# Performance work log

Measured on AMD Instinct MI355X. Metric: run time of the kernel, lower is better.

## Reference

```python
import jax, jax.numpy as jnp
import numpy as np

V_MIN = -10.0
V_MAX = 10.0
NUM_ATOMS = 51
ATOM_DELTA = (V_MAX - V_MIN) / (NUM_ATOMS - 1)
BS = 1_000_000


def setup_inputs() -> dict:
    key = jax.random.key(0)
    k1, k2 = jax.random.split(key)
    reward = jax.random.normal(k1, (BS,), dtype=jnp.float32) * 3.0
    probs = jax.random.uniform(k2, (BS, NUM_ATOMS), dtype=jnp.float32)
    atom_values = (V_MIN + ATOM_DELTA * jnp.arange(NUM_ATOMS)).astype(jnp.float32)
    return {"reward": reward, "probs": probs, "atom_values": atom_values}


def reference(reward, probs, atom_values):
    # Categorical (C51) Bellman projection, expressed as a scatter-add
    # instead of the original's dense [bs, A, A] projection matrix + bmm.
    bs, A = probs.shape
    # shifted & clamped atom support: [bs, A]
    new_vals = jnp.clip(atom_values[None, :] + reward[:, None], V_MIN, V_MAX)
    idx = (new_vals - V_MIN) / ATOM_DELTA           # fractional atom index
    lower = jnp.floor(idx)
    upper = jnp.ceil(idx)
    same = lower == upper                           # idx landed exactly on an atom
    l_coef = jnp.where(same, 1.0, upper - idx)      # original sets 1.0 when l == u
    u_coef = idx - lower                            # 0 when same
    li = lower.astype(jnp.int32)
    ui = upper.astype(jnp.int32)
    rows = jnp.broadcast_to(jnp.arange(bs)[:, None], (bs, A))
    out = jnp.zeros_like(probs)
    out = out.at[rows, li].add(l_coef * probs)
    out = out.at[rows, ui].add(u_coef * probs)
    return out
```

## Files before the change

### kernel.cpp

```cpp
#include <hip/hip_runtime.h>

#define NA 51
#define ROWS 64
#define GUARD 56
#define NDATA (ROWS * NA)
#define KCLAMP 52

__global__ __launch_bounds__(ROWS, 3) void c51_bellman_kernel(
    const float* __restrict__ reward,
    const float* __restrict__ probs,
    float* __restrict__ out,
    int bs)
{
    __shared__ float lds[GUARD + NDATA + GUARD];
    float* data = lds + GUARD;
    const int tid   = threadIdx.x;
    const int row0  = blockIdx.x * ROWS;
    const int nrows = min(ROWS, bs - row0);

    float s = 0.0f;
    if (tid < nrows) s = reward[row0 + tid] * 2.5f;

    if (nrows == ROWS) {
        const char* src = (const char*)(probs + (size_t)row0 * NA);
        #pragma unroll
        for (int t = 0; t < 12; ++t) {
            __builtin_amdgcn_global_load_lds(
                (const __attribute__((address_space(1))) void*)
                    (unsigned long long)(src + t * 1024 + tid * 16),
                (__attribute__((address_space(3))) void*)
                    (unsigned long long)(data + t * 256),
                16, 0, 0);
        }
        if (tid < 48) {
            const float4 v = *(const float4*)(src + 12288 + (size_t)tid * 16);
            *(float4*)(data + 3072 + tid * 4) = v;
        }
    } else {
        const int nelem = nrows * NA;
        for (int e = tid; e < nelem; e += ROWS)
            data[e] = probs[(size_t)row0 * NA + e];
    }
    asm volatile("s_waitcnt vmcnt(0) lgkmcnt(0)" ::: "memory");
    __builtin_amdgcn_sched_barrier(0);

    if (tid < nrows) {
        const float kf = floorf(s);
        const float f  = s - kf;
        int k = (int)kf;
        k = min(max(k, -KCLAMP), KCLAMP);

        const float* rp = data + tid * NA;

        float m_lo = 0.0f, m_hi = 0.0f;
        #pragma unroll
        for (int j = 0; j < NA; ++j) {
            const float pj = rp[j];
            const float t  = (float)j + s;
            if (t < 0.0f)  m_lo += pj;
            if (t > 50.0f) m_hi += pj;
        }

        const float* wb = data + tid * NA - k - 1;
        float w[52];
        #pragma unroll
        for (int m = 0; m < 52; ++m) w[m] = wb[m];

        float* wp = data + tid * NA;
        const float w1 = 1.0f - f;
        float prev = ((unsigned)(-k - 1) <= 50u) ? w[0] : 0.0f;
        #pragma unroll
        for (int i = 0; i < NA; ++i) {
            const float cur = ((unsigned)(i - k) <= 50u) ? w[i + 1] : 0.0f;
            float o;
            if (i == 0)           o = w1 * cur + m_lo;
            else if (i == NA - 1) o = ((f == 0.0f) ? cur : f * prev) + m_hi;
            else                  o = w1 * cur + f * prev;
            wp[i] = o;
            prev = cur;
        }
    }
    asm volatile("s_waitcnt lgkmcnt(0)" ::: "memory");
    __builtin_amdgcn_sched_barrier(0);

    if (nrows == ROWS) {
        float4* o4 = (float4*)(out + (size_t)row0 * NA);
        const float4* l4 = (const float4*)data;
        #pragma unroll
        for (int t = 0; t < 12; ++t) o4[t * 64 + tid] = l4[t * 64 + tid];
        if (tid < 48) o4[768 + tid] = l4[768 + tid];
    } else {
        const int nelem = nrows * NA;
        for (int e = tid; e < nelem; e += ROWS)
            out[(size_t)row0 * NA + e] = data[e];
    }
}

extern "C" void kernel_launch(void* const* d_in, const int* in_sizes, int n_in,
                              void* d_out, int out_size, void* d_ws, size_t ws_size,
                              hipStream_t stream) {
    const float* reward = (const float*)d_in[0];
    const float* probs  = (const float*)d_in[1];
    float* out = (float*)d_out;
    const int bs = in_sizes[0];

    const int blocks = (bs + ROWS - 1) / ROWS;
    c51_bellman_kernel<<<blocks, ROWS, 0, stream>>>(reward, probs, out, bs);
}
```

Measured before the change: 344.7 us.

## Drop LDS staging; load rows directly per thread and store nontemporally

```diff
diff --git a/kernel.cpp b/kernel.cpp
--- a/kernel.cpp
+++ b/kernel.cpp
@@ -1,99 +1,74 @@
 #include <hip/hip_runtime.h>
 
 #define NA 51
-#define ROWS 64
-#define GUARD 56
-#define NDATA (ROWS * NA)
+#define TPB 256
 #define KCLAMP 52
 
-__global__ __launch_bounds__(ROWS, 3) void c51_bellman_kernel(
+typedef float f4 __attribute__((ext_vector_type(4), aligned(4)));
+typedef float f2 __attribute__((ext_vector_type(2), aligned(4)));
+
+__global__ __launch_bounds__(TPB, 4) void c51_bellman_kernel(
     const float* __restrict__ reward,
     const float* __restrict__ probs,
     float* __restrict__ out,
     int bs)
 {
-    __shared__ float lds[GUARD + NDATA + GUARD];
-    float* data = lds + GUARD;
-    const int tid   = threadIdx.x;
-    const int row0  = blockIdx.x * ROWS;
-    const int nrows = min(ROWS, bs - row0);
+    const int r = blockIdx.x * TPB + threadIdx.x;
+    const bool edge = (blockIdx.x == 0) | (blockIdx.x == (int)gridDim.x - 1);
+    if (r >= bs) return;
 
-    float s = 0.0f;
-    if (tid < nrows) s = reward[row0 + tid] * 2.5f;
+    const float s  = reward[r] * 2.5f;
+    const float kf = floorf(s);
+    const float f  = s - kf;
+    int k = (int)kf;
+    k = min(max(k, -KCLAMP), KCLAMP);
 
-    if (nrows == ROWS) {
-        const char* src = (const char*)(probs + (size_t)row0 * NA);
+    const float* rp = probs + (size_t)r * NA;
+
+    float row[51];
+    #pragma unroll
+    for (int m = 0; m < 12; ++m) *(f4*)&row[4 * m] = *(const f4*)&rp[4 * m];
+    *(f2*)&row[48] = *(const f2*)&rp[48];
+    row[50] = rp[50];
+
+    float m_lo = 0.0f, m_hi = 0.0f;
+    #pragma unroll
+    for (int j = 0; j < NA; ++j) {
+        const float t = (float)j + s;
+        if (t < 0.0f)  m_lo += row[j];
+        if (t > 50.0f) m_hi += row[j];
+    }
+
+    float w[52];
+    if (!edge) {
+        const float* wb = rp - k - 1;
         #pragma unroll
-        for (int t = 0; t < 12; ++t) {
-            __builtin_amdgcn_global_load_lds(
-                (const __attribute__((address_space(1))) void*)
-                    (unsigned long long)(src + t * 1024 + tid * 16),
-                (__attribute__((address_space(3))) void*)
-                    (unsigned long long)(data + t * 256),
-                16, 0, 0);
-        }
-        if (tid < 48) {
-            const float4 v = *(const float4*)(src + 12288 + (size_t)tid * 16);
-            *(float4*)(data + 3072 + tid * 4) = v;
-        }
+        for (int m = 0; m < 13; ++m) *(f4*)&w[4 * m] = *(const f4*)&wb[4 * m];
     } else {
-        const int nelem = nrows * NA;
-        for (int e = tid; e < nelem; e += ROWS)
-            data[e] = probs[(size_t)row0 * NA + e];
+        #pragma unroll
+        for (int m = 0; m < 52; ++m)
+            w[m] = rp[min(max(m - k - 1, 0), NA - 1)];
     }
-    asm volatile("s_waitcnt vmcnt(0) lgkmcnt(0)" ::: "memory");
-    __builtin_amdgcn_sched_barrier(0);
 
-    if (tid < nrows) {
-        const float kf = floorf(s);
-        const float f  = s - kf;
-        int k = (int)kf;
-        k = min(max(k, -KCLAMP), KCLAMP);
+    const float w1 = 1.0f - f;
+    float prev = ((unsigned)(-k - 1) <= 50u) ? w[0] : 0.0f;
+    #pragma unroll
+    for (int i = 0; i < NA; ++i) {
+        const float cur = ((unsigned)(i - k) <= 50u) ? w[i + 1] : 0.0f;
+        float o;
+        if (i == 0)           o = w1 * cur + m_lo;
+        else if (i == NA - 1) o = ((f == 0.0f) ? cur : f * prev) + m_hi;
+        else                  o = w1 * cur + f * prev;
+        w[i] = o;
+        prev = cur;
+    }
 
-        const float* rp = data + tid * NA;
-
-        float m_lo = 0.0f, m_hi = 0.0f;
-        #pragma unroll
-        for (int j = 0; j < NA; ++j) {
-            const float pj = rp[j];
-            const float t  = (float)j + s;
-            if (t < 0.0f)  m_lo += pj;
-            if (t > 50.0f) m_hi += pj;
-        }
-
-        const float* wb = data + tid * NA - k - 1;
-        float w[52];
-        #pragma unroll
-        for (int m = 0; m < 52; ++m) w[m] = wb[m];
-
-        float* wp = data + tid * NA;
-        const float w1 = 1.0f - f;
-        float prev = ((unsigned)(-k - 1) <= 50u) ? w[0] : 0.0f;
-        #pragma unroll
-        for (int i = 0; i < NA; ++i) {
-            const float cur = ((unsigned)(i - k) <= 50u) ? w[i + 1] : 0.0f;
-            float o;
-            if (i == 0)           o = w1 * cur + m_lo;
-            else if (i == NA - 1) o = ((f == 0.0f) ? cur : f * prev) + m_hi;
-            else                  o = w1 * cur + f * prev;
-            wp[i] = o;
-            prev = cur;
-        }
-    }
-    asm volatile("s_waitcnt lgkmcnt(0)" ::: "memory");
-    __builtin_amdgcn_sched_barrier(0);
-
-    if (nrows == ROWS) {
-        float4* o4 = (float4*)(out + (size_t)row0 * NA);
-        const float4* l4 = (const float4*)data;
-        #pragma unroll
-        for (int t = 0; t < 12; ++t) o4[t * 64 + tid] = l4[t * 64 + tid];
-        if (tid < 48) o4[768 + tid] = l4[768 + tid];
-    } else {
-        const int nelem = nrows * NA;
-        for (int e = tid; e < nelem; e += ROWS)
-            out[(size_t)row0 * NA + e] = data[e];
-    }
+    float* op = out + (size_t)r * NA;
+    #pragma unroll
+    for (int m = 0; m < 12; ++m)
+        __builtin_nontemporal_store(*(const f4*)&w[4 * m], (f4*)&op[4 * m]);
+    __builtin_nontemporal_store(*(const f2*)&w[48], (f2*)&op[48]);
+    __builtin_nontemporal_store(w[50], &op[50]);
 }
 
 extern "C" void kernel_launch(void* const* d_in, const int* in_sizes, int n_in,
@@ -104,6 +79,6 @@
     float* out = (float*)d_out;
     const int bs = in_sizes[0];
 
-    const int blocks = (bs + ROWS - 1) / ROWS;
-    c51_bellman_kernel<<<blocks, ROWS, 0, stream>>>(reward, probs, out, bs);
+    const int blocks = (bs + TPB - 1) / TPB;
+    c51_bellman_kernel<<<blocks, TPB, 0, stream>>>(reward, probs, out, bs);
 }
```

After: 775.3 us. 2.25x slower.
